# Optimization experiments

Hardware: AMD Instinct MI355X
Metric: run time of the kernel (lower is better)

The kernel has to match this reference:

```python
import jax, jax.numpy as jnp
import numpy as np

LN_EPS = 1e-6  # flax.linen.LayerNorm default

def _layernorm(x, scale, bias):
    mu = jnp.mean(x, axis=-1, keepdims=True)
    var = jnp.mean(jnp.square(x - mu), axis=-1, keepdims=True)
    return (x - mu) * jax.lax.rsqrt(var + LN_EPS) * scale + bias

def setup_inputs() -> dict:
    key = jax.random.key(0)
    ks = jax.random.split(key, 16)
    N, D = 65536, 512
    W = 1024  # hidden width for all 4 layers
    def init_w(k, fan_in, fan_out):
        # lecun_normal (flax Dense default kernel init)
        return jax.random.normal(k, (fan_in, fan_out), jnp.float32) / np.sqrt(fan_in)
    return {
        "descriptors": jax.random.normal(ks[0], (N, D), jnp.float32),
        "W0": init_w(ks[1], D, W),
        "b0": jnp.zeros((W,), jnp.float32),
        "W1": init_w(ks[2], W, W),
        "g1": jnp.ones((W,), jnp.float32),
        "be1": jnp.zeros((W,), jnp.float32),
        "W2": init_w(ks[3], W, W),
        "g2": jnp.ones((W,), jnp.float32),
        "be2": jnp.zeros((W,), jnp.float32),
        "W3": init_w(ks[4], W, W),
        "g3": jnp.ones((W,), jnp.float32),
        "be3": jnp.zeros((W,), jnp.float32),
        "Wout": init_w(ks[5], W, 1),
        "bout": jnp.zeros((1,), jnp.float32),
    }

def reference(descriptors, W0, b0, W1, g1, be1, W2, g2, be2, W3, g3, be3, Wout, bout):
    # layer 0: Dense (with bias) -> relu
    h = jax.nn.relu(descriptors @ W0 + b0)  # [N, 1024]
    # hidden layers: bias-free Dense -> LayerNorm -> relu
    for Wk, gk, bk in ((W1, g1, be1), (W2, g2, be2), (W3, g3, be3)):
        h = jax.nn.relu(_layernorm(h @ Wk, gk, bk))
    # output: Dense(1) with bias -> relu
    return jax.nn.relu(h @ Wout + bout)  # [N, 1]
```

## Files before the change

### kernel.cpp

```cpp
#include <hip/hip_runtime.h>

typedef _Float16 f16;
typedef _Float16 f16x8 __attribute__((ext_vector_type(8)));
typedef float f32x16 __attribute__((ext_vector_type(16)));

#define TM 128
#define TN 256
#define BK 64

__device__ __forceinline__ void async_cp16(const void* g, void* l) {
  __builtin_amdgcn_global_load_lds(
      (const __attribute__((address_space(1))) void*)g,
      (__attribute__((address_space(3))) void*)l, 16, 0, 0);
}

template <int EPI>
__global__ __launch_bounds__(256, 2) void gemm_f16(
    const f16* __restrict__ A, const f16* __restrict__ Bt,
    const float* __restrict__ bias, f16* __restrict__ C,
    int M, int N, int K) {
  __shared__ alignas(16) f16 sA[TM][BK];
  __shared__ alignas(16) f16 sB[TN][BK];
  const int tid = threadIdx.x;
  const int lane = tid & 63;
  const int wave = tid >> 6;

  int mt, nt;
  if (gridDim.x == 4 && gridDim.y == 512) {
    const int id = blockIdx.y * 4 + blockIdx.x;
    nt = (id >> 3) & 3;
    mt = (id & 7) * 64 + (id >> 5);
  } else {
    nt = blockIdx.x;
    mt = blockIdx.y;
  }
  const long long bm = (long long)mt * TM;
  const long long bn = (long long)nt * TN;

  const int wm = (wave & 1) * 64;
  const int wn = (wave >> 1) * 128;
  const int l31 = lane & 31;
  const int half = lane >> 5;

  const f16* const Abase = A + bm * (long long)K;
  const f16* const Bbase = Bt + bn * (long long)K;
  int aOff[4], bOff[8];
#pragma unroll
  for (int i = 0; i < 4; ++i) {
    const int chunk = wave * 256 + i * 64 + lane;
    const int ml = chunk >> 3;
    const int kc = (chunk & 7) ^ (ml & 7);
    aOff[i] = ml * K + kc * 8;
  }
#pragma unroll
  for (int i = 0; i < 8; ++i) {
    const int chunk = wave * 512 + i * 64 + lane;
    const int ml = chunk >> 3;
    const int kc = (chunk & 7) ^ (ml & 7);
    bOff[i] = ml * K + kc * 8;
  }

  f32x16 acc[2][4] = {};

  const int kIters = K / BK;
  for (int kt = 0; kt < kIters; ++kt) {
    const int k0 = kt * BK;
#pragma unroll
    for (int i = 0; i < 4; ++i)
      async_cp16(Abase + aOff[i] + k0,
                 &sA[0][0] + (wave * 256 + i * 64) * 8);
#pragma unroll
    for (int i = 0; i < 8; ++i)
      async_cp16(Bbase + bOff[i] + k0,
                 &sB[0][0] + (wave * 512 + i * 64) * 8);
    __syncthreads();

#pragma unroll
    for (int s = 0; s < 4; ++s) {
      const int csw = ((s * 2 + half) ^ (lane & 7)) * 8;
      f16x8 af[2], bf[4];
#pragma unroll
      for (int i = 0; i < 2; ++i) af[i] = *(const f16x8*)&sA[wm + i * 32 + l31][csw];
#pragma unroll
      for (int j = 0; j < 4; ++j) bf[j] = *(const f16x8*)&sB[wn + j * 32 + l31][csw];
#pragma unroll
      for (int i = 0; i < 2; ++i)
#pragma unroll
        for (int j = 0; j < 4; ++j)
          acc[i][j] = __builtin_amdgcn_mfma_f32_32x32x16_f16(af[i], bf[j],
                                                             acc[i][j], 0, 0, 0);
    }
    __syncthreads();
  }

#pragma unroll
  for (int i = 0; i < 2; ++i)
#pragma unroll
    for (int j = 0; j < 4; ++j) {
      const long long colg = bn + wn + j * 32 + l31;
      float bval = 0.f;
      if (EPI == 0) bval = bias[colg];
#pragma unroll
      for (int reg = 0; reg < 16; ++reg) {
        const long long rowg =
            bm + wm + i * 32 + (reg & 3) + 8 * (reg >> 2) + 4 * half;
        float v = acc[i][j][reg];
        if (EPI == 0) v = fmaxf(v + bval, 0.f);
        C[rowg * N + colg] = (f16)v;
      }
    }
}

__global__ __launch_bounds__(256) void ln_relu_kernel(
    const f16* __restrict__ Y, const float* __restrict__ g,
    const float* __restrict__ b, f16* __restrict__ H) {
  const int lane = threadIdx.x & 63;
  const int wave = threadIdx.x >> 6;
  const long long row = (long long)blockIdx.x * 4 + wave;
  const f16* y = Y + row * 1024;
  float x[16];
  float s1 = 0.f, s2 = 0.f;
#pragma unroll
  for (int p = 0; p < 2; ++p) {
    f16x8 v = *(const f16x8*)(y + p * 512 + lane * 8);
#pragma unroll
    for (int e = 0; e < 8; ++e) {
      const float f = (float)v[e];
      x[p * 8 + e] = f;
      s1 += f;
      s2 += f * f;
    }
  }
#pragma unroll
  for (int off = 32; off >= 1; off >>= 1) {
    s1 += __shfl_xor(s1, off);
    s2 += __shfl_xor(s2, off);
  }
  const float mean = s1 * (1.f / 1024.f);
  const float var = fmaxf(s2 * (1.f / 1024.f) - mean * mean, 0.f);
  const float inv = rsqrtf(var + 1e-6f);
  f16* h = H + row * 1024;
#pragma unroll
  for (int p = 0; p < 2; ++p) {
    f16x8 o;
#pragma unroll
    for (int e = 0; e < 8; ++e) {
      const int c = p * 512 + lane * 8 + e;
      const float v = (x[p * 8 + e] - mean) * inv * g[c] + b[c];
      o[e] = (f16)fmaxf(v, 0.f);
    }
    *(f16x8*)(h + p * 512 + lane * 8) = o;
  }
}

__global__ __launch_bounds__(256) void ln_relu_out_kernel(
    const f16* __restrict__ Y, const float* __restrict__ g,
    const float* __restrict__ b, const float* __restrict__ Wout,
    const float* __restrict__ bout, float* __restrict__ out) {
  const int lane = threadIdx.x & 63;
  const int wave = threadIdx.x >> 6;
  const long long row = (long long)blockIdx.x * 4 + wave;
  const f16* y = Y + row * 1024;
  float x[16];
  float s1 = 0.f, s2 = 0.f;
#pragma unroll
  for (int p = 0; p < 2; ++p) {
    f16x8 v = *(const f16x8*)(y + p * 512 + lane * 8);
#pragma unroll
    for (int e = 0; e < 8; ++e) {
      const float f = (float)v[e];
      x[p * 8 + e] = f;
      s1 += f;
      s2 += f * f;
    }
  }
#pragma unroll
  for (int off = 32; off >= 1; off >>= 1) {
    s1 += __shfl_xor(s1, off);
    s2 += __shfl_xor(s2, off);
  }
  const float mean = s1 * (1.f / 1024.f);
  const float var = fmaxf(s2 * (1.f / 1024.f) - mean * mean, 0.f);
  const float inv = rsqrtf(var + 1e-6f);
  float dot = 0.f;
#pragma unroll
  for (int p = 0; p < 2; ++p) {
#pragma unroll
    for (int e = 0; e < 8; ++e) {
      const int c = p * 512 + lane * 8 + e;
      const float v = fmaxf((x[p * 8 + e] - mean) * inv * g[c] + b[c], 0.f);
      dot += v * Wout[c];
    }
  }
#pragma unroll
  for (int off = 32; off >= 1; off >>= 1) dot += __shfl_xor(dot, off);
  if (lane == 0) out[row] = fmaxf(dot + bout[0], 0.f);
}

__global__ __launch_bounds__(256) void cvt_f16_kernel(const float* __restrict__ X,
                                                      f16* __restrict__ Y,
                                                      long long n) {
  const long long i = ((long long)blockIdx.x * 256 + threadIdx.x) * 8;
  if (i >= n) return;
  const float4* X4 = (const float4*)(X + i);
  const float4 a = X4[0], c = X4[1];
  f16x8 o;
  o[0] = (f16)a.x; o[1] = (f16)a.y; o[2] = (f16)a.z; o[3] = (f16)a.w;
  o[4] = (f16)c.x; o[5] = (f16)c.y; o[6] = (f16)c.z; o[7] = (f16)c.w;
  *(f16x8*)(Y + i) = o;
}

__global__ __launch_bounds__(256) void transpose_cvt(const float* __restrict__ W,
                                                     f16* __restrict__ Wt, int K,
                                                     int N) {
  __shared__ float tile[64][65];
  const int bn = blockIdx.x * 64;
  const int bk = blockIdx.y * 64;
  const int tx = threadIdx.x & 63;
  const int ty = threadIdx.x >> 6;
#pragma unroll
  for (int i = 0; i < 64; i += 4)
    tile[ty + i][tx] = W[(long long)(bk + ty + i) * N + bn + tx];
  __syncthreads();
#pragma unroll
  for (int i = 0; i < 64; i += 4)
    Wt[(long long)(bn + ty + i) * K + bk + tx] = (f16)tile[tx][ty + i];
}

extern "C" void kernel_launch(void* const* d_in, const int* in_sizes, int n_in,
                              void* d_out, int out_size, void* d_ws, size_t ws_size,
                              hipStream_t stream) {
  const float* desc = (const float*)d_in[0];
  const float* W0 = (const float*)d_in[1];
  const float* b0 = (const float*)d_in[2];
  const float* W1 = (const float*)d_in[3];
  const float* g1 = (const float*)d_in[4];
  const float* be1 = (const float*)d_in[5];
  const float* W2 = (const float*)d_in[6];
  const float* g2 = (const float*)d_in[7];
  const float* be2 = (const float*)d_in[8];
  const float* W3 = (const float*)d_in[9];
  const float* g3 = (const float*)d_in[10];
  const float* be3 = (const float*)d_in[11];
  const float* Wout = (const float*)d_in[12];
  const float* bout = (const float*)d_in[13];
  float* out = (float*)d_out;

  const long long Nrows = 65536, D = 512, W = 1024;
  char* p = (char*)d_ws;
  f16* descH = (f16*)p; p += Nrows * D * sizeof(f16);
  f16* Wt0 = (f16*)p;   p += D * W * sizeof(f16);
  f16* Wt1 = (f16*)p;   p += W * W * sizeof(f16);
  f16* Wt2 = (f16*)p;   p += W * W * sizeof(f16);
  f16* Wt3 = (f16*)p;   p += W * W * sizeof(f16);
  f16* H = (f16*)p;     p += Nrows * W * sizeof(f16);
  f16* Y = (f16*)p;     p += Nrows * W * sizeof(f16);
  (void)ws_size; (void)in_sizes; (void)n_in; (void)out_size;

  cvt_f16_kernel<<<(int)(Nrows * D / 8 / 256), 256, 0, stream>>>(desc, descH,
                                                                 Nrows * D);
  transpose_cvt<<<dim3(W / 64, D / 64), 256, 0, stream>>>(W0, Wt0, (int)D, (int)W);
  transpose_cvt<<<dim3(W / 64, W / 64), 256, 0, stream>>>(W1, Wt1, (int)W, (int)W);
  transpose_cvt<<<dim3(W / 64, W / 64), 256, 0, stream>>>(W2, Wt2, (int)W, (int)W);
  transpose_cvt<<<dim3(W / 64, W / 64), 256, 0, stream>>>(W3, Wt3, (int)W, (int)W);

  dim3 ggrid(W / TN, Nrows / TM);
  gemm_f16<0><<<ggrid, 256, 0, stream>>>(descH, Wt0, b0, H, (int)Nrows, (int)W, (int)D);

  gemm_f16<1><<<ggrid, 256, 0, stream>>>(H, Wt1, nullptr, Y, (int)Nrows, (int)W, (int)W);
  ln_relu_kernel<<<(int)(Nrows / 4), 256, 0, stream>>>(Y, g1, be1, H);

  gemm_f16<1><<<ggrid, 256, 0, stream>>>(H, Wt2, nullptr, Y, (int)Nrows, (int)W, (int)W);
  ln_relu_kernel<<<(int)(Nrows / 4), 256, 0, stream>>>(Y, g2, be2, H);

  gemm_f16<1><<<ggrid, 256, 0, stream>>>(H, Wt3, nullptr, Y, (int)Nrows, (int)W, (int)W);
  ln_relu_out_kernel<<<(int)(Nrows / 4), 256, 0, stream>>>(Y, g3, be3, Wout, bout, out);
}
```

Measured before the change: 886.8 us.

## Rewrite GEMM as 256x256 tile, 8-wave, double-buffered pipelined MFMA kernel

Replaces the 128x256 single-buffered GEMM with a 256x256 tile kernel using 512 threads, 16x16x32 MFMAs, and a two-stage LDS double buffer split into 32-wide k-halves. Global-to-LDS loads for future k-steps are issued between MFMA phases, with explicit vmcnt waits and barriers, so memory transfers overlap compute. It also raises MFMA priority during compute phases and changes the tile-swizzled block ordering. The larger tile improves reuse, but it doubles LDS use to 128KB per block and increases register pressure, which may limit occupancy.

New measurement: 940.9 us. 6.1% more time.

```diff
diff --git a/kernel.cpp b/kernel.cpp
--- a/kernel.cpp
+++ b/kernel.cpp
@@ -2,11 +2,7 @@
 
 typedef _Float16 f16;
 typedef _Float16 f16x8 __attribute__((ext_vector_type(8)));
-typedef float f32x16 __attribute__((ext_vector_type(16)));
-
-#define TM 128
-#define TN 256
-#define BK 64
+typedef float f32x4 __attribute__((ext_vector_type(4)));
 
 __device__ __forceinline__ void async_cp16(const void* g, void* l) {
   __builtin_amdgcn_global_load_lds(
@@ -14,101 +10,131 @@
       (__attribute__((address_space(3))) void*)l, 16, 0, 0);
 }
 
+#define BARRIER()               \
+  __builtin_amdgcn_s_barrier(); \
+  __builtin_amdgcn_sched_barrier(0)
+
 template <int EPI>
-__global__ __launch_bounds__(256, 2) void gemm_f16(
+__global__ __launch_bounds__(512, 2) void gemm256(
     const f16* __restrict__ A, const f16* __restrict__ Bt,
     const float* __restrict__ bias, f16* __restrict__ C,
     int M, int N, int K) {
-  __shared__ alignas(16) f16 sA[TM][BK];
-  __shared__ alignas(16) f16 sB[TN][BK];
+  __shared__ alignas(16) f16 sA[2][2][256][32];
+  __shared__ alignas(16) f16 sB[2][2][256][32];
   const int tid = threadIdx.x;
   const int lane = tid & 63;
   const int wave = tid >> 6;
+  const int wm = (wave >> 2) * 128;
+  const int wn = (wave & 3) * 64;
+  const int l15 = lane & 15;
+  const int swz = (((lane >> 4) ^ (lane & 3)) << 3);
 
   int mt, nt;
-  if (gridDim.x == 4 && gridDim.y == 512) {
+  if (gridDim.x == 4 && gridDim.y == 256) {
     const int id = blockIdx.y * 4 + blockIdx.x;
-    nt = (id >> 3) & 3;
-    mt = (id & 7) * 64 + (id >> 5);
+    const int j = id >> 3;
+    mt = (id & 7) * 32 + (j >> 2);
+    nt = j & 3;
   } else {
     nt = blockIdx.x;
     mt = blockIdx.y;
   }
-  const long long bm = (long long)mt * TM;
-  const long long bn = (long long)nt * TN;
-
-  const int wm = (wave & 1) * 64;
-  const int wn = (wave >> 1) * 128;
-  const int l31 = lane & 31;
-  const int half = lane >> 5;
-
+  const long long bm = (long long)mt * 256;
+  const long long bn = (long long)nt * 256;
   const f16* const Abase = A + bm * (long long)K;
   const f16* const Bbase = Bt + bn * (long long)K;
-  int aOff[4], bOff[8];
-#pragma unroll
-  for (int i = 0; i < 4; ++i) {
-    const int chunk = wave * 256 + i * 64 + lane;
-    const int ml = chunk >> 3;
-    const int kc = (chunk & 7) ^ (ml & 7);
-    aOff[i] = ml * K + kc * 8;
-  }
-#pragma unroll
-  for (int i = 0; i < 8; ++i) {
-    const int chunk = wave * 512 + i * 64 + lane;
-    const int ml = chunk >> 3;
-    const int kc = (chunk & 7) ^ (ml & 7);
-    bOff[i] = ml * K + kc * 8;
-  }
-
-  f32x16 acc[2][4] = {};
-
-  const int kIters = K / BK;
-  for (int kt = 0; kt < kIters; ++kt) {
-    const int k0 = kt * BK;
-#pragma unroll
-    for (int i = 0; i < 4; ++i)
-      async_cp16(Abase + aOff[i] + k0,
-                 &sA[0][0] + (wave * 256 + i * 64) * 8);
-#pragma unroll
-    for (int i = 0; i < 8; ++i)
-      async_cp16(Bbase + bOff[i] + k0,
-                 &sB[0][0] + (wave * 512 + i * 64) * 8);
-    __syncthreads();
-
-#pragma unroll
-    for (int s = 0; s < 4; ++s) {
-      const int csw = ((s * 2 + half) ^ (lane & 7)) * 8;
-      f16x8 af[2], bf[4];
-#pragma unroll
-      for (int i = 0; i < 2; ++i) af[i] = *(const f16x8*)&sA[wm + i * 32 + l31][csw];
-#pragma unroll
-      for (int j = 0; j < 4; ++j) bf[j] = *(const f16x8*)&sB[wn + j * 32 + l31][csw];
-#pragma unroll
-      for (int i = 0; i < 2; ++i)
-#pragma unroll
-        for (int j = 0; j < 4; ++j)
-          acc[i][j] = __builtin_amdgcn_mfma_f32_32x32x16_f16(af[i], bf[j],
-                                                             acc[i][j], 0, 0, 0);
-    }
-    __syncthreads();
-  }
-
-#pragma unroll
-  for (int i = 0; i < 2; ++i)
-#pragma unroll
-    for (int j = 0; j < 4; ++j) {
-      const long long colg = bn + wn + j * 32 + l31;
-      float bval = 0.f;
-      if (EPI == 0) bval = bias[colg];
-#pragma unroll
-      for (int reg = 0; reg < 16; ++reg) {
-        const long long rowg =
-            bm + wm + i * 32 + (reg & 3) + 8 * (reg >> 2) + 4 * half;
-        float v = acc[i][j][reg];
+
+  int gOff[2];
+#pragma unroll
+  for (int i = 0; i < 2; ++i) {
+    const int cu = (wave * 2 + i) * 64 + lane;
+    const int row = cu >> 2;
+    gOff[i] = row * K + (((cu & 3) ^ (row & 3)) << 3);
+  }
+  auto stage = [&](const f16* gbase, f16* lbase, int k0) {
+#pragma unroll
+    for (int i = 0; i < 2; ++i)
+      async_cp16(gbase + gOff[i] + k0, lbase + (wave * 2 + i) * 512);
+  };
+
+  f32x4 acc[8][4] = {};
+  const int nT = K >> 6;
+
+#define READ_A(KS)                            \
+  _Pragma("unroll") for (int m = 0; m < 8; ++m) \
+      af[m] = *(const f16x8*)&sA[cur][KS][wm + m * 16 + l15][swz];
+#define READ_B(KS, NH)                        \
+  _Pragma("unroll") for (int n = 0; n < 2; ++n) \
+      bf[n] = *(const f16x8*)&sB[cur][KS][wn + (NH) * 32 + n * 16 + l15][swz];
+#define PHASE_MFMA(NH)                                                 \
+  __builtin_amdgcn_s_setprio(1);                                       \
+  _Pragma("unroll") for (int m = 0; m < 8; ++m)                        \
+      _Pragma("unroll") for (int n = 0; n < 2; ++n)                    \
+          acc[m][(NH) * 2 + n] = __builtin_amdgcn_mfma_f32_16x16x32_f16( \
+              af[m], bf[n], acc[m][(NH) * 2 + n], 0, 0, 0);            \
+  __builtin_amdgcn_s_setprio(0)
+
+  stage(Abase, &sA[0][0][0][0], 0);
+  stage(Abase, &sA[0][1][0][0], 32);
+  stage(Bbase, &sB[0][0][0][0], 0);
+  stage(Bbase, &sB[0][1][0][0], 32);
+  stage(Abase, &sA[1][0][0][0], 64);
+  stage(Bbase, &sB[1][0][0][0], 64);
+  stage(Abase, &sA[1][1][0][0], 96);
+  asm volatile("s_waitcnt vmcnt(6)" ::: "memory");
+  BARRIER();
+
+  for (int t = 0; t < nT; ++t) {
+    const int cur = t & 1;
+    const int nxt = cur ^ 1;
+    f16x8 af[8], bf[2];
+    READ_A(0);
+    READ_B(0, 0);
+    if (t + 1 < nT) stage(Bbase, &sB[nxt][1][0][0], (t + 1) * 64 + 32);
+    BARRIER();
+    PHASE_MFMA(0);
+    BARRIER();
+    READ_B(0, 1);
+    if (t + 2 < nT) stage(Abase, &sA[cur][0][0][0], (t + 2) * 64);
+    BARRIER();
+    PHASE_MFMA(1);
+    BARRIER();
+    READ_A(1);
+    READ_B(1, 0);
+    if (t + 2 < nT) stage(Bbase, &sB[cur][0][0][0], (t + 2) * 64);
+    BARRIER();
+    PHASE_MFMA(0);
+    BARRIER();
+    READ_B(1, 1);
+    if (t + 2 < nT) stage(Abase, &sA[cur][1][0][0], (t + 2) * 64 + 32);
+    BARRIER();
+    PHASE_MFMA(1);
+    if (t + 2 < nT)
+      asm volatile("s_waitcnt vmcnt(6)" ::: "memory");
+    else if (t + 2 == nT)
+      asm volatile("s_waitcnt vmcnt(0)" ::: "memory");
+    BARRIER();
+  }
+#undef READ_A
+#undef READ_B
+#undef PHASE_MFMA
+
+#pragma unroll
+  for (int n = 0; n < 4; ++n) {
+    const long long col = bn + wn + n * 16 + l15;
+    float bval = 0.f;
+    if (EPI == 0) bval = bias[col];
+#pragma unroll
+    for (int m = 0; m < 8; ++m) {
+      const long long rowb = bm + wm + m * 16 + (lane >> 4) * 4;
+#pragma unroll
+      for (int r = 0; r < 4; ++r) {
+        float v = acc[m][n][r];
         if (EPI == 0) v = fmaxf(v + bval, 0.f);
-        C[rowg * N + colg] = (f16)v;
+        C[(rowb + r) * N + col] = (f16)v;
       }
     }
+  }
 }
 
 __global__ __launch_bounds__(256) void ln_relu_kernel(
@@ -264,15 +290,15 @@
   transpose_cvt<<<dim3(W / 64, W / 64), 256, 0, stream>>>(W2, Wt2, (int)W, (int)W);
   transpose_cvt<<<dim3(W / 64, W / 64), 256, 0, stream>>>(W3, Wt3, (int)W, (int)W);
 
-  dim3 ggrid(W / TN, Nrows / TM);
-  gemm_f16<0><<<ggrid, 256, 0, stream>>>(descH, Wt0, b0, H, (int)Nrows, (int)W, (int)D);
-
-  gemm_f16<1><<<ggrid, 256, 0, stream>>>(H, Wt1, nullptr, Y, (int)Nrows, (int)W, (int)W);
+  dim3 ggrid(W / 256, Nrows / 256);
+  gemm256<0><<<ggrid, 512, 0, stream>>>(descH, Wt0, b0, H, (int)Nrows, (int)W, (int)D);
+
+  gemm256<1><<<ggrid, 512, 0, stream>>>(H, Wt1, nullptr, Y, (int)Nrows, (int)W, (int)W);
   ln_relu_kernel<<<(int)(Nrows / 4), 256, 0, stream>>>(Y, g1, be1, H);
 
-  gemm_f16<1><<<ggrid, 256, 0, stream>>>(H, Wt2, nullptr, Y, (int)Nrows, (int)W, (int)W);
+  gemm256<1><<<ggrid, 512, 0, stream>>>(H, Wt2, nullptr, Y, (int)Nrows, (int)W, (int)W);
   ln_relu_kernel<<<(int)(Nrows / 4), 256, 0, stream>>>(Y, g2, be2, H);
 
-  gemm_f16<1><<<ggrid, 256, 0, stream>>>(H, Wt3, nullptr, Y, (int)Nrows, (int)W, (int)W);
+  gemm256<1><<<ggrid, 512, 0, stream>>>(H, Wt3, nullptr, Y, (int)Nrows, (int)W, (int)W);
   ln_relu_out_kernel<<<(int)(Nrows / 4), 256, 0, stream>>>(Y, g3, be3, Wout, bout, out);
 }
```

## Fuse LayerNorm into GEMM A-loads via atomic row statistics, drop standalone passes

Applied to the files above, without the earlier changes.

The GEMM epilogue now accumulates per-row sum and sum-of-squares with atomics. The next GEMM applies LayerNorm and ReLU while loading its A tile through registers, so the separate ln_relu kernels are gone. The first GEMM reads the fp32 descriptors directly and converts them to f16 in registers, which removes the separate conversion pass. This saves several full read/write passes over 65536x1024 activations. The cost is losing the async global-to-LDS copy on the A path and adding atomic traffic in the epilogue.

Result: slower. 1.061 ms (+19.7%).

```diff
diff --git a/kernel.cpp b/kernel.cpp
--- a/kernel.cpp
+++ b/kernel.cpp
@@ -14,11 +14,13 @@
       (__attribute__((address_space(3))) void*)l, 16, 0, 0);
 }
 
-template <int EPI>
+template <int LNA, int EPI, int STATS>
 __global__ __launch_bounds__(256, 2) void gemm_f16(
-    const f16* __restrict__ A, const f16* __restrict__ Bt,
-    const float* __restrict__ bias, f16* __restrict__ C,
-    int M, int N, int K) {
+    const f16* __restrict__ Af16, const float* __restrict__ Af32,
+    const f16* __restrict__ Bt, const float* __restrict__ bias,
+    const float* __restrict__ lnStats, const float* __restrict__ lnG,
+    const float* __restrict__ lnB, float* __restrict__ statsOut,
+    f16* __restrict__ C, int M, int N, int K) {
   __shared__ alignas(16) f16 sA[TM][BK];
   __shared__ alignas(16) f16 sB[TN][BK];
   const int tid = threadIdx.x;
@@ -42,7 +44,8 @@
   const int l31 = lane & 31;
   const int half = lane >> 5;
 
-  const f16* const Abase = A + bm * (long long)K;
+  const f16* const Abase = Af16 + bm * (long long)K;
+  const float* const A32base = Af32 ? (Af32 + bm * (long long)K) : nullptr;
   const f16* const Bbase = Bt + bn * (long long)K;
   int aOff[4], bOff[8];
 #pragma unroll
@@ -60,19 +63,66 @@
     bOff[i] = ml * K + kc * 8;
   }
 
+  float rMu[4], rInv[4];
+  int aKc8[4];
+  if (LNA == 1) {
+#pragma unroll
+    for (int i = 0; i < 4; ++i) {
+      const int chunk = wave * 256 + i * 64 + lane;
+      const int ml = chunk >> 3;
+      aKc8[i] = ((chunk & 7) ^ (ml & 7)) * 8;
+      const long long r = bm + ml;
+      const float s1 = lnStats[2 * r];
+      const float s2 = lnStats[2 * r + 1];
+      const float mu = s1 * (1.f / 1024.f);
+      const float var = fmaxf(s2 * (1.f / 1024.f) - mu * mu, 0.f);
+      rMu[i] = mu;
+      rInv[i] = rsqrtf(var + 1e-6f);
+    }
+  }
+
   f32x16 acc[2][4] = {};
 
   const int kIters = K / BK;
   for (int kt = 0; kt < kIters; ++kt) {
     const int k0 = kt * BK;
-#pragma unroll
-    for (int i = 0; i < 4; ++i)
-      async_cp16(Abase + aOff[i] + k0,
-                 &sA[0][0] + (wave * 256 + i * 64) * 8);
+    if (LNA == 0) {
+#pragma unroll
+      for (int i = 0; i < 4; ++i)
+        async_cp16(Abase + aOff[i] + k0, &sA[0][0] + (wave * 256 + i * 64) * 8);
+    } else if (LNA == 1) {
+#pragma unroll
+      for (int i = 0; i < 4; ++i) {
+        const f16x8 yv = *(const f16x8*)(Abase + aOff[i] + k0);
+        const int c0 = aKc8[i] + k0;
+        float gv[8], bv[8];
+        *(float4*)(gv) = *(const float4*)(lnG + c0);
+        *(float4*)(gv + 4) = *(const float4*)(lnG + c0 + 4);
+        *(float4*)(bv) = *(const float4*)(lnB + c0);
+        *(float4*)(bv + 4) = *(const float4*)(lnB + c0 + 4);
+        f16x8 o;
+#pragma unroll
+        for (int e = 0; e < 8; ++e) {
+          const float x = (float)yv[e];
+          o[e] = (f16)fmaxf((x - rMu[i]) * rInv[i] * gv[e] + bv[e], 0.f);
+        }
+        *(f16x8*)(&sA[0][0] + (wave * 256 + i * 64 + lane) * 8) = o;
+      }
+    } else {
+#pragma unroll
+      for (int i = 0; i < 4; ++i) {
+        float xv[8];
+        *(float4*)(xv) = *(const float4*)(A32base + aOff[i] + k0);
+        *(float4*)(xv + 4) = *(const float4*)(A32base + aOff[i] + k0 + 4);
+        f16x8 o;
+#pragma unroll
+        for (int e = 0; e < 8; ++e) o[e] = (f16)xv[e];
+        *(f16x8*)(&sA[0][0] + (wave * 256 + i * 64 + lane) * 8) = o;
+      }
+    }
 #pragma unroll
     for (int i = 0; i < 8; ++i)
-      async_cp16(Bbase + bOff[i] + k0,
-                 &sB[0][0] + (wave * 512 + i * 64) * 8);
+      async_cp16(Bbase + bOff[i] + k0, &sB[0][0] + (wave * 512 + i * 64) * 8);
     __syncthreads();
 
 #pragma unroll
@@ -109,47 +159,31 @@
         C[rowg * N + colg] = (f16)v;
       }
     }
-}
-
-__global__ __launch_bounds__(256) void ln_relu_kernel(
-    const f16* __restrict__ Y, const float* __restrict__ g,
-    const float* __restrict__ b, f16* __restrict__ H) {
-  const int lane = threadIdx.x & 63;
-  const int wave = threadIdx.x >> 6;
-  const long long row = (long long)blockIdx.x * 4 + wave;
-  const f16* y = Y + row * 1024;
-  float x[16];
-  float s1 = 0.f, s2 = 0.f;
-#pragma unroll
-  for (int p = 0; p < 2; ++p) {
-    f16x8 v = *(const f16x8*)(y + p * 512 + lane * 8);
-#pragma unroll
-    for (int e = 0; e < 8; ++e) {
-      const float f = (float)v[e];
-      x[p * 8 + e] = f;
-      s1 += f;
-      s2 += f * f;
-    }
-  }
-#pragma unroll
-  for (int off = 32; off >= 1; off >>= 1) {
-    s1 += __shfl_xor(s1, off);
-    s2 += __shfl_xor(s2, off);
-  }
-  const float mean = s1 * (1.f / 1024.f);
-  const float var = fmaxf(s2 * (1.f / 1024.f) - mean * mean, 0.f);
-  const float inv = rsqrtf(var + 1e-6f);
-  f16* h = H + row * 1024;
-#pragma unroll
-  for (int p = 0; p < 2; ++p) {
-    f16x8 o;
-#pragma unroll
-    for (int e = 0; e < 8; ++e) {
-      const int c = p * 512 + lane * 8 + e;
-      const float v = (x[p * 8 + e] - mean) * inv * g[c] + b[c];
-      o[e] = (f16)fmaxf(v, 0.f);
-    }
-    *(f16x8*)(h + p * 512 + lane * 8) = o;
+
+  if (STATS) {
+#pragma unroll
+    for (int i = 0; i < 2; ++i)
+#pragma unroll
+      for (int reg = 0; reg < 16; ++reg) {
+        float s1 = 0.f, s2 = 0.f;
+#pragma unroll
+        for (int j = 0; j < 4; ++j) {
+          const float v = acc[i][j][reg];
+          s1 += v;
+          s2 += v * v;
+        }
+#pragma unroll
+        for (int off = 16; off >= 1; off >>= 1) {
+          s1 += __shfl_xor(s1, off);
+          s2 += __shfl_xor(s2, off);
+        }
+        if (l31 == 0) {
+          const long long rowg =
+              bm + wm + i * 32 + (reg & 3) + 8 * (reg >> 2) + 4 * half;
+          atomicAdd(statsOut + 2 * rowg, s1);
+          atomicAdd(statsOut + 2 * rowg + 1, s2);
+        }
+      }
   }
 }
 
@@ -197,19 +231,6 @@
   if (lane == 0) out[row] = fmaxf(dot + bout[0], 0.f);
 }
 
-__global__ __launch_bounds__(256) void cvt_f16_kernel(const float* __restrict__ X,
-                                                      f16* __restrict__ Y,
-                                                      long long n) {
-  const long long i = ((long long)blockIdx.x * 256 + threadIdx.x) * 8;
-  if (i >= n) return;
-  const float4* X4 = (const float4*)(X + i);
-  const float4 a = X4[0], c = X4[1];
-  f16x8 o;
-  o[0] = (f16)a.x; o[1] = (f16)a.y; o[2] = (f16)a.z; o[3] = (f16)a.w;
-  o[4] = (f16)c.x; o[5] = (f16)c.y; o[6] = (f16)c.z; o[7] = (f16)c.w;
-  *(f16x8*)(Y + i) = o;
-}
-
 __global__ __launch_bounds__(256) void transpose_cvt(const float* __restrict__ W,
                                                      f16* __restrict__ Wt, int K,
                                                      int N) {
@@ -225,6 +246,12 @@
 #pragma unroll
   for (int i = 0; i < 64; i += 4)
     Wt[(long long)(bn + ty + i) * K + bk + tx] = (f16)tile[tx][ty + i];
+}
+
+__global__ __launch_bounds__(256) void zero_kernel(float4* __restrict__ p,
+                                                   int n4) {
+  const int i = blockIdx.x * 256 + threadIdx.x;
+  if (i < n4) p[i] = float4{0.f, 0.f, 0.f, 0.f};
 }
 
 extern "C" void kernel_launch(void* const* d_in, const int* in_sizes, int n_in,
@@ -248,31 +275,41 @@
 
   const long long Nrows = 65536, D = 512, W = 1024;
   char* p = (char*)d_ws;
-  f16* descH = (f16*)p; p += Nrows * D * sizeof(f16);
   f16* Wt0 = (f16*)p;   p += D * W * sizeof(f16);
   f16* Wt1 = (f16*)p;   p += W * W * sizeof(f16);
   f16* Wt2 = (f16*)p;   p += W * W * sizeof(f16);
   f16* Wt3 = (f16*)p;   p += W * W * sizeof(f16);
   f16* H = (f16*)p;     p += Nrows * W * sizeof(f16);
   f16* Y = (f16*)p;     p += Nrows * W * sizeof(f16);
+  float* stats1 = (float*)p; p += Nrows * 2 * sizeof(float);
+  float* stats2 = (float*)p; p += Nrows * 2 * sizeof(float);
   (void)ws_size; (void)in_sizes; (void)n_in; (void)out_size;
 
-  cvt_f16_kernel<<<(int)(Nrows * D / 8 / 256), 256, 0, stream>>>(desc, descH,
-                                                                 Nrows * D);
+  zero_kernel<<<(int)(Nrows * 4 / 4 / 256), 256, 0, stream>>>((float4*)stats1,
+                                                              (int)(Nrows * 4 / 4));
   transpose_cvt<<<dim3(W / 64, D / 64), 256, 0, stream>>>(W0, Wt0, (int)D, (int)W);
   transpose_cvt<<<dim3(W / 64, W / 64), 256, 0, stream>>>(W1, Wt1, (int)W, (int)W);
   transpose_cvt<<<dim3(W / 64, W / 64), 256, 0, stream>>>(W2, Wt2, (int)W, (int)W);
   transpose_cvt<<<dim3(W / 64, W / 64), 256, 0, stream>>>(W3, Wt3, (int)W, (int)W);
 
   dim3 ggrid(W / TN, Nrows / TM);
-  gemm_f16<0><<<ggrid, 256, 0, stream>>>(descH, Wt0, b0, H, (int)Nrows, (int)W, (int)D);
-
-  gemm_f16<1><<<ggrid, 256, 0, stream>>>(H, Wt1, nullptr, Y, (int)Nrows, (int)W, (int)W);
-  ln_relu_kernel<<<(int)(Nrows / 4), 256, 0, stream>>>(Y, g1, be1, H);
-
-  gemm_f16<1><<<ggrid, 256, 0, stream>>>(H, Wt2, nullptr, Y, (int)Nrows, (int)W, (int)W);
-  ln_relu_kernel<<<(int)(Nrows / 4), 256, 0, stream>>>(Y, g2, be2, H);
-
-  gemm_f16<1><<<ggrid, 256, 0, stream>>>(H, Wt3, nullptr, Y, (int)Nrows, (int)W, (int)W);
-  ln_relu_out_kernel<<<(int)(Nrows / 4), 256, 0, stream>>>(Y, g3, be3, Wout, bout, out);
-}
+
+  gemm_f16<2, 0, 0><<<ggrid, 256, 0, stream>>>(
+      nullptr, desc, Wt0, b0, nullptr, nullptr, nullptr, nullptr, H,
+      (int)Nrows, (int)W, (int)D);
+
+  gemm_f16<0, 1, 1><<<ggrid, 256, 0, stream>>>(
+      H, nullptr, Wt1, nullptr, nullptr, nullptr, nullptr, stats1, Y,
+      (int)Nrows, (int)W, (int)W);
+
+  gemm_f16<1, 1, 1><<<ggrid, 256, 0, stream>>>(
+      Y, nullptr, Wt2, nullptr, stats1, g1, be1, stats2, H,
+      (int)Nrows, (int)W, (int)W);
+
+  gemm_f16<1, 1, 0><<<ggrid, 256, 0, stream>>>(
+      H, nullptr, Wt3, nullptr, stats2, g2, be2, nullptr, Y,
+      (int)Nrows, (int)W, (int)W);
+
+  ln_relu_out_kernel<<<(int)(Nrows / 4), 256, 0, stream>>>(Y, g3, be3, Wout,
+                                                           bout, out);
+}
```
